# Kernel optimization log

Measured on AMD Instinct MI355X. Metric: run time of the kernel, lower is better.

The kernel has to match this reference:

```python
import math
import jax, jax.numpy as jnp
import numpy as np

H = 8  # num_heads

def _layernorm(x, scale, bias, eps=1e-5):
    m = x.mean(-1, keepdims=True)
    v = x.var(-1, keepdims=True)
    return (x - m) / jnp.sqrt(v + eps) * scale + bias

def setup_inputs() -> dict:
    key = jax.random.key(0)
    ks = jax.random.split(key, 12)
    B, C, P, D, G = 8, 32, 256, 256, 512
    n = jax.random.normal
    return {
        "qz": n(ks[0], (B, C, P, D), dtype=jnp.float32),
        "unary": n(ks[1], (B, C, P, D), dtype=jnp.float32),
        # per-sample condition-instantiated factors; scaled ~1/sqrt(D) so attn logits are sane
        "time_u": n(ks[2], (B, D, D), dtype=jnp.float32) * 0.06,
        "time_v": n(ks[3], (B, D, D), dtype=jnp.float32) * 0.06,
        "channel_u": n(ks[4], (B, D, D), dtype=jnp.float32) * 0.06,
        "channel_v": n(ks[5], (B, D, D), dtype=jnp.float32) * 0.06,
        "topic_binary": n(ks[6], (B, G, D), dtype=jnp.float32) * 0.02,
        "norm_scale": jnp.ones((D,), jnp.float32),
        "norm_bias": jnp.zeros((D,), jnp.float32),
        "gate_w": n(ks[7], (D, D), dtype=jnp.float32) * 0.02,
        "gate_b": jnp.zeros((D,), jnp.float32),
        "out_w1": n(ks[8], (D, D), dtype=jnp.float32) * 0.02,
        "out_b1": jnp.zeros((D,), jnp.float32),
        "out_w2": n(ks[9], (D, D), dtype=jnp.float32) * 0.02,
        "out_b2": jnp.zeros((D,), jnp.float32),
    }

def reference(qz, unary, time_u, time_v, channel_u, channel_v, topic_binary,
              norm_scale, norm_bias, gate_w, gate_b, out_w1, out_b1, out_w2, out_b2):
    B, C, P, D = qz.shape
    R = D // H
    inv_sqrt_r = 1.0 / math.sqrt(R)

    qz_n = _layernorm(qz, norm_scale, norm_bias)

    def heads(x, w):  # [B,C,P,D] x [B,D,D] -> [B,C,P,H,R]
        return jnp.einsum('bcpd,bod->bcpo', x, w).reshape(B, C, P, H, R)

    # --- time-factor message: attention over P within each (b, c, h) ---
    qu = heads(qz_n, time_u).transpose(0, 1, 3, 2, 4)   # [B,C,H,P,R]
    qv = heads(qz_n, time_v).transpose(0, 1, 3, 2, 4)
    attn_t = jax.nn.softmax(jnp.einsum('bchpr,bchqr->bchpq', qu, qv) * inv_sqrt_r, axis=-1)
    m_t = jnp.einsum('bchpq,bcqd->bchpd', attn_t, qz_n).mean(axis=2)  # [B,C,P,D]

    # --- channel-factor message: attention over C within each (b, p, h) ---
    qu = heads(qz_n, channel_u).transpose(0, 2, 3, 1, 4)  # [B,P,H,C,R]
    qv = heads(qz_n, channel_v).transpose(0, 2, 3, 1, 4)
    attn_c = jax.nn.softmax(jnp.einsum('bphcr,bphfr->bphcf', qu, qv) * inv_sqrt_r, axis=-1)
    qzp = qz_n.transpose(0, 2, 1, 3)                      # [B,P,C,D]
    m_c = jnp.einsum('bphcf,bpfd->bphcd', attn_c, qzp).mean(axis=2).transpose(0, 2, 1, 3)

    # --- topic-modeling binary factor with AbsNormalize (relu + L1-normalize) ---
    qg = jax.nn.relu(jnp.einsum('bcpd,bgd->bcpg', qz_n, topic_binary))
    qg = qg / jnp.maximum(qg.sum(axis=-1, keepdims=True), 1e-6)
    m_g = jnp.einsum('bcpg,bgd->bcpd', qg, topic_binary)

    # --- gated residual update ---
    gate = jax.nn.sigmoid(qz @ gate_w.T + gate_b)
    qz2 = gate * qz + (1.0 - gate) * (unary + m_t + m_c + m_g)

    # --- output MLP with shared LayerNorm ---
    h = _layernorm(qz2, norm_scale, norm_bias)
    h = jax.nn.gelu(h @ out_w1.T + out_b1, approximate=False) @ out_w2.T + out_b2
    return qz2 + h
```

## Files before the change

kernel.cpp:

```cpp
#include <hip/hip_runtime.h>
#include <math.h>

namespace {

constexpr float INV_SQRT_R = 0.17677669529663689f;

typedef __attribute__((ext_vector_type(8))) __bf16 bf16x8;
typedef __attribute__((ext_vector_type(4))) float f32x4;

static __device__ __forceinline__ f32x4 MF(bf16x8 a, bf16x8 b, f32x4 c) {
    return __builtin_amdgcn_mfma_f32_16x16x32_bf16(a, b, c, 0, 0, 0);
}


__global__ __launch_bounds__(256) void prep_kernel(
    const float* __restrict__ time_u, const float* __restrict__ time_v,
    const float* __restrict__ chan_u, const float* __restrict__ chan_v,
    const float* __restrict__ topic, const float* __restrict__ gate_w,
    const float* __restrict__ w1, const float* __restrict__ w2,
    __bf16* __restrict__ wtime, __bf16* __restrict__ wchan,
    __bf16* __restrict__ topicb, __bf16* __restrict__ topicTb,
    __bf16* __restrict__ gwF, __bf16* __restrict__ w1F, __bf16* __restrict__ w2F)
{
    __shared__ __bf16 tile[32][34];
    const int blk = blockIdx.x;
    const int t = threadIdx.x;
    if (blk < 2048) {
        const int q = blk >> 9, r = blk & 511;
        const float* src; __bf16* dst; int dstOff;
        if (q == 0)      { src = time_u; dst = wtime; dstOff = 0; }
        else if (q == 1) { src = time_v; dst = wtime; dstOff = 65536; }
        else if (q == 2) { src = chan_u; dst = wchan; dstOff = 0; }
        else             { src = chan_v; dst = wchan; dstOff = 65536; }
        int i = (r * 256 + t) * 4;
        float4 v = *(const float4*)(src + i);
        int o = (i >> 16) * 131072 + dstOff + (i & 65535);
        dst[o + 0] = (__bf16)v.x; dst[o + 1] = (__bf16)v.y;
        dst[o + 2] = (__bf16)v.z; dst[o + 3] = (__bf16)v.w;
    } else if (blk < 3072) {
        int i = ((blk - 2048) * 256 + t) * 4;
        float4 v = *(const float4*)(topic + i);
        topicb[i + 0] = (__bf16)v.x; topicb[i + 1] = (__bf16)v.y;
        topicb[i + 2] = (__bf16)v.z; topicb[i + 3] = (__bf16)v.w;
    } else if (blk < 4096) {
        const int idx = blk - 3072;
        const int r0 = (idx & 15) * 32;
        const int c0 = ((idx >> 4) & 7) * 32;
        const size_t bz = idx >> 7;
        const float* src = topic + bz * 131072;
        __bf16* dst = topicTb + bz * 131072;
        const int tx = t & 31, ty = t >> 5;
        #pragma unroll
        for (int i = 0; i < 32; i += 8)
            tile[ty + i][tx] = (__bf16)src[(size_t)(r0 + ty + i) * 256 + c0 + tx];
        __syncthreads();
        #pragma unroll
        for (int i = 0; i < 32; i += 8)
            dst[(size_t)(c0 + ty + i) * 512 + r0 + tx] = tile[tx][ty + i];
    } else {
        const int w = (blk - 4096) >> 6;
        const int r = (blk - 4096) & 63;
        const float* src = (w == 0) ? gate_w : ((w == 1) ? w1 : w2);
        __bf16* dstB = (w == 0) ? gwF : ((w == 1) ? w1F : w2F);
        int i = (r * 256 + t) * 4;
        float4 v = *(const float4*)(src + i);
        const int n = i >> 8, k = i & 255;
        __bf16* dst = dstB + (k >> 5) * 8192 + n * 32 + (k & 31);
        dst[0] = (__bf16)v.x; dst[1] = (__bf16)v.y; dst[2] = (__bf16)v.z; dst[3] = (__bf16)v.w;
    }
}

__global__ __launch_bounds__(256) void ln_kernel(
    const float* __restrict__ x, const float* __restrict__ sc,
    const float* __restrict__ bi, __bf16* __restrict__ y)
{
    const size_t row = blockIdx.x;
    const int t = threadIdx.x;
    const float v = x[row * 256 + t];
    float s = v, s2 = v * v;
    #pragma unroll
    for (int o = 32; o > 0; o >>= 1) {
        s  += __shfl_xor(s, o);
        s2 += __shfl_xor(s2, o);
    }
    __shared__ float ps[4], ps2[4];
    if ((t & 63) == 0) { ps[t >> 6] = s; ps2[t >> 6] = s2; }
    __syncthreads();
    const float S  = ps[0] + ps[1] + ps[2] + ps[3];
    const float S2 = ps2[0] + ps2[1] + ps2[2] + ps2[3];
    const float mean = S * (1.0f / 256.0f);
    const float var  = S2 * (1.0f / 256.0f) - mean * mean;
    const float inv  = 1.0f / sqrtf(var + 1e-5f);
    y[row * 256 + t] = (__bf16)((v - mean) * inv * sc[t] + bi[t]);
}

__global__ __launch_bounds__(256) void tpose_frag_kernel(
    const __bf16* __restrict__ src, __bf16* __restrict__ dst)
{
    const size_t bz = blockIdx.z;
    src += bz * 65536;
    dst += bz * 65536;
    __shared__ __bf16 tile[32][34];
    const int r0 = blockIdx.x * 32, c0 = blockIdx.y * 32;
    const int tx = threadIdx.x & 31, ty = threadIdx.x >> 5;
    #pragma unroll
    for (int i = 0; i < 32; i += 8)
        tile[ty + i][tx] = src[(size_t)(r0 + ty + i) * 256 + c0 + tx];
    __syncthreads();
    #pragma unroll
    for (int i = 0; i < 32; i += 8)
        dst[(r0 >> 5) * 8192 + (c0 + ty + i) * 32 + tx] = tile[tx][ty + i];
}

__global__ __launch_bounds__(256) void mgemm_kernel(
    const __bf16* __restrict__ A, const __bf16* __restrict__ Bm, __bf16* __restrict__ Cout,
    int K, size_t aStride, size_t bStride,
    size_t s_b, size_t s_c, size_t s_p, size_t s_w, size_t s_h)
{
    const int bb = blockIdx.z;
    const int m0 = blockIdx.x * 64;
    const int n0 = blockIdx.y * 256;
    const __bf16* Ab = A + (size_t)bb * aStride;
    const __bf16* Bb = Bm + (size_t)bb * bStride;
    __shared__ __align__(16) __bf16 As[64][40];
    __shared__ __align__(16) __bf16 Bs[256][40];
    const int t = threadIdx.x;
    const int lane = t & 63;
    const int wid = t >> 6;
    const int l15 = lane & 15, lg = lane >> 4;

    f32x4 acc[4][4] = {};

    for (int k0 = 0; k0 < K; k0 += 32) {
        {
            const int row = t >> 2, k8 = (t & 3) << 3;
            *(bf16x8*)&As[row][k8] = *(const bf16x8*)(Ab + (size_t)(m0 + row) * K + k0 + k8);
        }
        #pragma unroll
        for (int s = 0; s < 4; ++s) {
            const int slot = s * 256 + t;
            const int row = slot >> 2, k8 = (slot & 3) << 3;
            *(bf16x8*)&Bs[row][k8] = *(const bf16x8*)(Bb + (size_t)(n0 + row) * K + k0 + k8);
        }
        __syncthreads();
        bf16x8 af[4], bfr[4];
        #pragma unroll
        for (int i = 0; i < 4; ++i)
            af[i] = *(const bf16x8*)&As[i * 16 + l15][lg * 8];
        #pragma unroll
        for (int j = 0; j < 4; ++j)
            bfr[j] = *(const bf16x8*)&Bs[wid * 64 + j * 16 + l15][lg * 8];
        #pragma unroll
        for (int i = 0; i < 4; ++i)
            #pragma unroll
            for (int j = 0; j < 4; ++j)
                acc[i][j] = MF(af[i], bfr[j], acc[i][j]);
        __syncthreads();
    }

    #pragma unroll
    for (int j = 0; j < 4; ++j) {
        const int n = n0 + wid * 64 + j * 16 + l15;
        const size_t offn = (size_t)(n >> 8) * s_w + (size_t)((n >> 5) & 7) * s_h + (n & 31);
        #pragma unroll
        for (int i = 0; i < 4; ++i) {
            #pragma unroll
            for (int r = 0; r < 4; ++r) {
                const int m = m0 + i * 16 + lg * 4 + r;
                const size_t off = (size_t)bb * s_b + (size_t)(m >> 8) * s_c
                                 + (size_t)(m & 255) * s_p + offn;
                Cout[off] = (__bf16)acc[i][j][r];
            }
        }
    }
}

__global__ __launch_bounds__(256) void time_attn_mt_kernel(
    const __bf16* __restrict__ qu, const __bf16* __restrict__ qv,
    const __bf16* __restrict__ qznTF, __bf16* __restrict__ m_t)
{
    const int bc = blockIdx.x;
    const int p0 = blockIdx.y * 64;
    const __bf16* quB = qu + (size_t)bc * 65536;
    const __bf16* qvB = qv + (size_t)bc * 65536;
    const __bf16* BTF = qznTF + (size_t)bc * 65536;
    __shared__ __align__(16) __bf16 R1[16896];
    __bf16* Us  = R1;
    __bf16* Vs  = R1 + 2560;
    __bf16* aL  = R1;
    const int t = threadIdx.x;
    const int lane = t & 63;
    const int wid = t >> 6;
    const int l15 = lane & 15, lg = lane >> 4;

    f32x4 acc[16] = {};

    for (int h = 0; h < 8; ++h) {
        const __bf16* quH = quB + h * 8192;
        const __bf16* qvH = qvB + h * 8192;
        __syncthreads();
        {
            const int row = t >> 2, k8 = (t & 3) << 3;
            *(bf16x8*)&Us[row * 40 + k8] = *(const bf16x8*)(quH + (size_t)(p0 + row) * 32 + k8);
        }
        #pragma unroll
        for (int i = 0; i < 4; ++i) {
            const int slot = i * 256 + t;
            const int row = slot >> 2, k8 = (slot & 3) << 3;
            *(bf16x8*)&Vs[row * 40 + k8] = *(const bf16x8*)(qvH + (size_t)row * 32 + k8);
        }
        __syncthreads();

        f32x4 s[16];
        bf16x8 a = *(const bf16x8*)&Us[(wid * 16 + l15) * 40 + lg * 8];
        #pragma unroll
        for (int j = 0; j < 16; ++j) {
            bf16x8 bfr = *(const bf16x8*)&Vs[(j * 16 + l15) * 40 + lg * 8];
            s[j] = MF(a, bfr, (f32x4){0.f, 0.f, 0.f, 0.f});
        }

        #pragma unroll
        for (int r = 0; r < 4; ++r) {
            float e[16];
            float sum = 0.0f;
            #pragma unroll
            for (int j = 0; j < 16; ++j) {
                e[j] = __expf(s[j][r] * INV_SQRT_R);
                sum += e[j];
            }
            sum += __shfl_xor(sum, 1);
            sum += __shfl_xor(sum, 2);
            sum += __shfl_xor(sum, 4);
            sum += __shfl_xor(sum, 8);
            const float inv = 0.125f / sum;
            #pragma unroll
            for (int j = 0; j < 16; ++j) acc[j][r] += e[j] * inv;
        }
    }

    __syncthreads();
    #pragma unroll
    for (int r = 0; r < 4; ++r) {
        const int row = wid * 16 + lg * 4 + r;
        #pragma unroll
        for (int j = 0; j < 16; ++j)
            aL[row * 264 + j * 16 + l15] = (__bf16)acc[j][r];
    }
    __syncthreads();

    f32x4 acc2[4][4] = {};
    #pragma unroll
    for (int k0 = 0; k0 < 256; k0 += 32) {
        bf16x8 af[4], bfr[4];
        #pragma unroll
        for (int i = 0; i < 4; ++i)
            af[i] = *(const bf16x8*)&aL[(i * 16 + l15) * 264 + k0 + lg * 8];
        #pragma unroll
        for (int j = 0; j < 4; ++j)
            bfr[j] = *(const bf16x8*)(BTF + (k0 >> 5) * 8192 + (wid * 64 + j * 16 + l15) * 32 + lg * 8);
        #pragma unroll
        for (int i = 0; i < 4; ++i)
            #pragma unroll
            for (int j = 0; j < 4; ++j)
                acc2[i][j] = MF(af[i], bfr[j], acc2[i][j]);
    }
    #pragma unroll
    for (int i = 0; i < 4; ++i)
        #pragma unroll
        for (int j = 0; j < 4; ++j) {
            const int d = wid * 64 + j * 16 + l15;
            #pragma unroll
            for (int r = 0; r < 4; ++r) {
                const int p = p0 + i * 16 + lg * 4 + r;
                m_t[(size_t)bc * 65536 + (size_t)p * 256 + d] = (__bf16)acc2[i][j][r];
            }
        }
}

__global__ __launch_bounds__(256) void chan_fused_kernel(
    const __bf16* __restrict__ quc, const __bf16* __restrict__ qvc,
    const __bf16* __restrict__ qzn, __bf16* __restrict__ m_c)
{
    const int bp = blockIdx.x;
    const int b = bp >> 8, p = bp & 255;
    const __bf16* quB = quc + (size_t)bp * 8192;
    const __bf16* qvB = qvc + (size_t)bp * 8192;
    __shared__ __align__(16) __bf16 QU[20480];
    __shared__ float ab[32 * 33];
    __bf16* qus = QU;
    __bf16* qvs = QU + 10240;
    const int t = threadIdx.x;

    float btr[32];
    #pragma unroll
    for (int f = 0; f < 32; ++f)
        btr[f] = (float)qzn[((size_t)(b * 32 + f) * 256 + p) * 256 + t];

    #pragma unroll
    for (int i = 0; i < 4; ++i) {
        int fi = i * 256 + t;
        int e = fi << 3;
        int h = e >> 10, cc = (e >> 5) & 31, r = e & 31;
        int base = (h * 32 + cc) * 40 + r;
        *(bf16x8*)&qus[base] = *(const bf16x8*)(quB + e);
        *(bf16x8*)&qvs[base] = *(const bf16x8*)(qvB + e);
    }
    __syncthreads();
    const int c = t >> 3, j = t & 7;
    float acc[4] = {0.f, 0.f, 0.f, 0.f};
    for (int h = 0; h < 8; ++h) {
        float qur[32];
        #pragma unroll
        for (int u = 0; u < 4; ++u) {
            bf16x8 q8 = *(const bf16x8*)&qus[(h * 32 + c) * 40 + u * 8];
            #pragma unroll
            for (int e2 = 0; e2 < 8; ++e2) qur[u * 8 + e2] = (float)q8[e2];
        }
        float s[4];
        #pragma unroll
        for (int jj = 0; jj < 4; ++jj) {
            int f = j * 4 + jj;
            float a = 0.f;
            #pragma unroll
            for (int u = 0; u < 4; ++u) {
                bf16x8 v8 = *(const bf16x8*)&qvs[(h * 32 + f) * 40 + u * 8];
                #pragma unroll
                for (int e2 = 0; e2 < 8; ++e2) a += qur[u * 8 + e2] * (float)v8[e2];
            }
            s[jj] = a * INV_SQRT_R;
        }
        float mx = fmaxf(fmaxf(s[0], s[1]), fmaxf(s[2], s[3]));
        mx = fmaxf(mx, __shfl_xor(mx, 1));
        mx = fmaxf(mx, __shfl_xor(mx, 2));
        mx = fmaxf(mx, __shfl_xor(mx, 4));
        float e0x = __expf(s[0] - mx), e1x = __expf(s[1] - mx);
        float e2x = __expf(s[2] - mx), e3x = __expf(s[3] - mx);
        float sum = e0x + e1x + e2x + e3x;
        sum += __shfl_xor(sum, 1);
        sum += __shfl_xor(sum, 2);
        sum += __shfl_xor(sum, 4);
        float inv = 0.125f / sum;
        acc[0] += e0x * inv; acc[1] += e1x * inv; acc[2] += e2x * inv; acc[3] += e3x * inv;
    }
    #pragma unroll
    for (int jj = 0; jj < 4; ++jj) ab[c * 33 + j * 4 + jj] = acc[jj];
    __syncthreads();
    #pragma unroll 2
    for (int c2 = 0; c2 < 32; c2 += 2) {
        float a0 = 0.f, a1 = 0.f;
        #pragma unroll
        for (int f = 0; f < 32; ++f) {
            float v = btr[f];
            a0 += ab[c2 * 33 + f] * v;
            a1 += ab[(c2 + 1) * 33 + f] * v;
        }
        size_t off = ((size_t)(b * 32 + c2) * 256 + p) * 256 + t;
        m_c[off] = (__bf16)a0;
        m_c[off + 65536] = (__bf16)a1;
    }
}

__global__ __launch_bounds__(256, 2) void topic_fused_kernel(
    const __bf16* __restrict__ qzn, const __bf16* __restrict__ topicb,
    const __bf16* __restrict__ topicTb, __bf16* __restrict__ m_g)
{
    const int bb = blockIdx.z;
    const int m0 = blockIdx.x * 32;
    const __bf16* Ab = qzn + (size_t)bb * 2097152;
    const __bf16* B1 = topicb + (size_t)bb * 131072;
    const __bf16* B2 = topicTb + (size_t)bb * 131072;
    __shared__ __align__(16) __bf16 As[32][40];
    __shared__ __align__(16) __bf16 Bs[512][40];
    __shared__ __align__(16) __bf16 Ps[32][520];
    __shared__ float rsInv[32];
    const int t = threadIdx.x;
    const int lane = t & 63, wid = t >> 6;
    const int l15 = lane & 15, lg = lane >> 4;

    f32x4 acc[2][8] = {};
    for (int k0 = 0; k0 < 256; k0 += 32) {
        if (t < 128) {
            const int row = t >> 2, k8 = (t & 3) << 3;
            *(bf16x8*)&As[row][k8] = *(const bf16x8*)(Ab + (size_t)(m0 + row) * 256 + k0 + k8);
        }
        #pragma unroll
        for (int s = 0; s < 8; ++s) {
            const int slot = s * 256 + t;
            const int row = slot >> 2, k8 = (slot & 3) << 3;
            *(bf16x8*)&Bs[row][k8] = *(const bf16x8*)(B1 + (size_t)row * 256 + k0 + k8);
        }
        __syncthreads();
        bf16x8 af0 = *(const bf16x8*)&As[l15][lg * 8];
        bf16x8 af1 = *(const bf16x8*)&As[16 + l15][lg * 8];
        #pragma unroll
        for (int j = 0; j < 8; ++j) {
            bf16x8 b8 = *(const bf16x8*)&Bs[wid * 128 + j * 16 + l15][lg * 8];
            acc[0][j] = MF(af0, b8, acc[0][j]);
            acc[1][j] = MF(af1, b8, acc[1][j]);
        }
        __syncthreads();
    }
    #pragma unroll
    for (int i = 0; i < 2; ++i)
        #pragma unroll
        for (int j = 0; j < 8; ++j) {
            const int n = wid * 128 + j * 16 + l15;
            #pragma unroll
            for (int r = 0; r < 4; ++r)
                Ps[i * 16 + lg * 4 + r][n] = (__bf16)fmaxf(acc[i][j][r], 0.0f);
        }
    __syncthreads();
    {
        const int row = t >> 3, seg = t & 7;
        float s = 0.0f;
        #pragma unroll
        for (int u = 0; u < 8; ++u) {
            bf16x8 v = *(const bf16x8*)&Ps[row][seg * 64 + u * 8];
            #pragma unroll
            for (int e = 0; e < 8; ++e) s += (float)v[e];
        }
        s += __shfl_xor(s, 1);
        s += __shfl_xor(s, 2);
        s += __shfl_xor(s, 4);
        if (seg == 0) rsInv[row] = 1.0f / fmaxf(s, 1e-6f);
    }
    __syncthreads();
    f32x4 acc2[2][4] = {};
    for (int k0 = 0; k0 < 512; k0 += 32) {
        #pragma unroll
        for (int s = 0; s < 4; ++s) {
            const int slot = s * 256 + t;
            const int row = slot >> 2, k8 = (slot & 3) << 3;
            *(bf16x8*)&Bs[row][k8] = *(const bf16x8*)(B2 + (size_t)row * 512 + k0 + k8);
        }
        __syncthreads();
        bf16x8 af0 = *(const bf16x8*)&Ps[l15][k0 + lg * 8];
        bf16x8 af1 = *(const bf16x8*)&Ps[16 + l15][k0 + lg * 8];
        #pragma unroll
        for (int j = 0; j < 4; ++j) {
            bf16x8 b8 = *(const bf16x8*)&Bs[wid * 64 + j * 16 + l15][lg * 8];
            acc2[0][j] = MF(af0, b8, acc2[0][j]);
            acc2[1][j] = MF(af1, b8, acc2[1][j]);
        }
        __syncthreads();
    }
    #pragma unroll
    for (int i = 0; i < 2; ++i)
        #pragma unroll
        for (int j = 0; j < 4; ++j) {
            const int n = wid * 64 + j * 16 + l15;
            #pragma unroll
            for (int r = 0; r < 4; ++r) {
                const int ml = i * 16 + lg * 4 + r;
                m_g[(size_t)bb * 2097152 + (size_t)(m0 + ml) * 256 + n]
                    = (__bf16)(acc2[i][j][r] * rsInv[ml]);
            }
        }
}

__global__ __launch_bounds__(256) void mega_kernel(
    const float* __restrict__ qz, const float* __restrict__ unary,
    const __bf16* __restrict__ m_t, const __bf16* __restrict__ m_c,
    const __bf16* __restrict__ m_g,
    const __bf16* __restrict__ gwF, const float* __restrict__ gate_b,
    const __bf16* __restrict__ w1F, const float* __restrict__ b1,
    const __bf16* __restrict__ w2F, const float* __restrict__ b2,
    const float* __restrict__ nsc, const float* __restrict__ nbi,
    float* __restrict__ outp)
{
    const int m0 = blockIdx.x * 64;
    __shared__ __align__(16) __bf16 hL[64][264];
    __shared__ float lnp[64][8];
    const int t = threadIdx.x;
    const int lane = t & 63, wid = t >> 6;
    const int l15 = lane & 15, lg = lane >> 4;

    #pragma unroll
    for (int s = 0; s < 8; ++s) {
        const int slot = s * 256 + t;
        const int row = slot >> 5;
        const int k8 = (slot & 31) << 3;
        const float* src = qz + (size_t)(m0 + row) * 256 + k8;
        float4 v0 = *(const float4*)src;
        float4 v1 = *(const float4*)(src + 4);
        bf16x8 pk;
        pk[0] = (__bf16)v0.x; pk[1] = (__bf16)v0.y; pk[2] = (__bf16)v0.z; pk[3] = (__bf16)v0.w;
        pk[4] = (__bf16)v1.x; pk[5] = (__bf16)v1.y; pk[6] = (__bf16)v1.z; pk[7] = (__bf16)v1.w;
        *(bf16x8*)&hL[row][k8] = pk;
    }
    __syncthreads();

    f32x4 acc[4][4] = {};
    #pragma unroll
    for (int k0 = 0; k0 < 256; k0 += 32) {
        bf16x8 af[4], bfr[4];
        #pragma unroll
        for (int i = 0; i < 4; ++i) af[i] = *(const bf16x8*)&hL[i * 16 + l15][k0 + lg * 8];
        #pragma unroll
        for (int j = 0; j < 4; ++j)
            bfr[j] = *(const bf16x8*)(gwF + (k0 >> 5) * 8192 + (wid * 64 + j * 16 + l15) * 32 + lg * 8);
        #pragma unroll
        for (int i = 0; i < 4; ++i)
            #pragma unroll
            for (int j = 0; j < 4; ++j)
                acc[i][j] = MF(af[i], bfr[j], acc[i][j]);
    }

    f32x4 z2[4][4];
    #pragma unroll
    for (int i = 0; i < 4; ++i) {
        #pragma unroll
        for (int r = 0; r < 4; ++r) {
            const int rr = i * 16 + lg * 4 + r;
            float s = 0.0f, s2 = 0.0f;
            #pragma unroll
            for (int j = 0; j < 4; ++j) {
                const int n = wid * 64 + j * 16 + l15;
                const size_t off = (size_t)(m0 + rr) * 256 + n;
                float g = 1.0f / (1.0f + __expf(-(acc[i][j][r] + gate_b[n])));
                float rest = unary[off] + (float)m_t[off] + (float)m_c[off] + (float)m_g[off];
                float v = g * (float)hL[rr][n] + (1.0f - g) * rest;
                z2[i][j][r] = v;
                s += v; s2 += v * v;
            }
            s  += __shfl_xor(s, 1);  s  += __shfl_xor(s, 2);
            s  += __shfl_xor(s, 4);  s  += __shfl_xor(s, 8);
            s2 += __shfl_xor(s2, 1); s2 += __shfl_xor(s2, 2);
            s2 += __shfl_xor(s2, 4); s2 += __shfl_xor(s2, 8);
            if (l15 == 0) {
                lnp[rr][wid * 2 + 0] = s;
                lnp[rr][wid * 2 + 1] = s2;
            }
        }
    }
    __syncthreads();
    #pragma unroll
    for (int i = 0; i < 4; ++i) {
        #pragma unroll
        for (int r = 0; r < 4; ++r) {
            const int rr = i * 16 + lg * 4 + r;
            float S  = lnp[rr][0] + lnp[rr][2] + lnp[rr][4] + lnp[rr][6];
            float S2 = lnp[rr][1] + lnp[rr][3] + lnp[rr][5] + lnp[rr][7];
            float mean = S * (1.0f / 256.0f);
            float var  = S2 * (1.0f / 256.0f) - mean * mean;
            float inv  = 1.0f / sqrtf(var + 1e-5f);
            #pragma unroll
            for (int j = 0; j < 4; ++j) {
                const int n = wid * 64 + j * 16 + l15;
                hL[rr][n] = (__bf16)((z2[i][j][r] - mean) * inv * nsc[n] + nbi[n]);
            }
        }
    }
    __syncthreads();

    f32x4 acc2[4][4] = {};
    #pragma unroll
    for (int k0 = 0; k0 < 256; k0 += 32) {
        bf16x8 af[4], bfr[4];
        #pragma unroll
        for (int i = 0; i < 4; ++i) af[i] = *(const bf16x8*)&hL[i * 16 + l15][k0 + lg * 8];
        #pragma unroll
        for (int j = 0; j < 4; ++j)
            bfr[j] = *(const bf16x8*)(w1F + (k0 >> 5) * 8192 + (wid * 64 + j * 16 + l15) * 32 + lg * 8);
        #pragma unroll
        for (int i = 0; i < 4; ++i)
            #pragma unroll
            for (int j = 0; j < 4; ++j)
                acc2[i][j] = MF(af[i], bfr[j], acc2[i][j]);
    }
    __syncthreads();
    #pragma unroll
    for (int i = 0; i < 4; ++i)
        #pragma unroll
        for (int j = 0; j < 4; ++j) {
            const int n = wid * 64 + j * 16 + l15;
            const float bn = b1[n];
            #pragma unroll
            for (int r = 0; r < 4; ++r) {
                float x = acc2[i][j][r] + bn;
                hL[i * 16 + lg * 4 + r][n] = (__bf16)(0.5f * x * (1.0f + erff(x * 0.7071067811865475f)));
            }
        }
    __syncthreads();

    f32x4 acc3[4][4] = {};
    #pragma unroll
    for (int k0 = 0; k0 < 256; k0 += 32) {
        bf16x8 af[4], bfr[4];
        #pragma unroll
        for (int i = 0; i < 4; ++i) af[i] = *(const bf16x8*)&hL[i * 16 + l15][k0 + lg * 8];
        #pragma unroll
        for (int j = 0; j < 4; ++j)
            bfr[j] = *(const bf16x8*)(w2F + (k0 >> 5) * 8192 + (wid * 64 + j * 16 + l15) * 32 + lg * 8);
        #pragma unroll
        for (int i = 0; i < 4; ++i)
            #pragma unroll
            for (int j = 0; j < 4; ++j)
                acc3[i][j] = MF(af[i], bfr[j], acc3[i][j]);
    }
    #pragma unroll
    for (int i = 0; i < 4; ++i)
        #pragma unroll
        for (int j = 0; j < 4; ++j) {
            const int n = wid * 64 + j * 16 + l15;
            const float bn = b2[n];
            #pragma unroll
            for (int r = 0; r < 4; ++r) {
                const size_t off = (size_t)(m0 + i * 16 + lg * 4 + r) * 256 + n;
                outp[off] = z2[i][j][r] + acc3[i][j][r] + bn;
            }
        }
}

}

extern "C" void kernel_launch(void* const* d_in, const int* in_sizes, int n_in,
                              void* d_out, int out_size, void* d_ws, size_t ws_size,
                              hipStream_t stream)
{
    (void)in_sizes; (void)n_in; (void)out_size; (void)ws_size;
    const float* qz     = (const float*)d_in[0];
    const float* unary  = (const float*)d_in[1];
    const float* time_u = (const float*)d_in[2];
    const float* time_v = (const float*)d_in[3];
    const float* chan_u = (const float*)d_in[4];
    const float* chan_v = (const float*)d_in[5];
    const float* topic  = (const float*)d_in[6];
    const float* nsc    = (const float*)d_in[7];
    const float* nbi    = (const float*)d_in[8];
    const float* gate_w = (const float*)d_in[9];
    const float* gate_b = (const float*)d_in[10];
    const float* w1     = (const float*)d_in[11];
    const float* b1     = (const float*)d_in[12];
    const float* w2     = (const float*)d_in[13];
    const float* b2     = (const float*)d_in[14];

    char* base = (char*)d_ws;
    __bf16* qzn_b  = (__bf16*)base;
    __bf16* pool   = (__bf16*)(base + (32ull << 20));
    __bf16* wtime  = pool;
    __bf16* wchan  = pool + 1048576;
    __bf16* topicb = pool + 2097152;
    __bf16* topicTb= pool + 3145728;
    __bf16* gwF    = pool + 4194304;
    __bf16* w1F    = pool + 4259840;
    __bf16* w2F    = pool + 4325376;
    __bf16* Blo    = (__bf16*)(base + (64ull << 20));
    __bf16* Bhi    = (__bf16*)(base + (96ull << 20));
    __bf16* qu_t   = Blo;
    __bf16* qv_t   = Bhi;
    __bf16* qu_c   = Blo;
    __bf16* qv_c   = Bhi;
    __bf16* m_g    = Blo;
    __bf16* qznTF  = (__bf16*)(base + (128ull << 20));
    __bf16* m_c    = qznTF;
    __bf16* m_t    = (__bf16*)(base + (160ull << 20));
    float*  OUTF   = (float*)d_out;

    dim3 blk(256);

    prep_kernel<<<4288, blk, 0, stream>>>(
        time_u, time_v, chan_u, chan_v, topic, gate_w, w1, w2,
        wtime, wchan, topicb, topicTb, gwF, w1F, w2F);

    ln_kernel<<<65536, blk, 0, stream>>>(qz, nsc, nbi, qzn_b);
    tpose_frag_kernel<<<dim3(8, 8, 256), blk, 0, stream>>>(qzn_b, qznTF);

    mgemm_kernel<<<dim3(128, 2, 8), blk, 0, stream>>>(
        qzn_b, wtime, qu_t, 256, 2097152, 131072,
        2097152, 65536, 32, 16777216, 8192);

    time_attn_mt_kernel<<<dim3(256, 4), blk, 0, stream>>>(qu_t, qv_t, qznTF, m_t);

    mgemm_kernel<<<dim3(128, 2, 8), blk, 0, stream>>>(
        qzn_b, wchan, qu_c, 256, 2097152, 131072,
        2097152, 32, 8192, 16777216, 1024);

    chan_fused_kernel<<<2048, blk, 0, stream>>>(qu_c, qv_c, qzn_b, m_c);

    topic_fused_kernel<<<dim3(256, 1, 8), blk, 0, stream>>>(qzn_b, topicb, topicTb, m_g);

    mega_kernel<<<1024, blk, 0, stream>>>(
        qz, unary, m_t, m_c, m_g,
        gwF, gate_b, w1F, b1, w2F, b2, nsc, nbi, OUTF);
}
```

Measured before the change: 483.6 us.

## Fuse time attention and channel projection GEMM into one interleaved launch

```diff
diff --git a/kernel.cpp b/kernel.cpp
--- a/kernel.cpp
+++ b/kernel.cpp
@@ -175,106 +175,168 @@
     }
 }
 
-__global__ __launch_bounds__(256) void time_attn_mt_kernel(
+__global__ __launch_bounds__(256) void mid_kernel(
     const __bf16* __restrict__ qu, const __bf16* __restrict__ qv,
-    const __bf16* __restrict__ qznTF, __bf16* __restrict__ m_t)
-{
-    const int bc = blockIdx.x;
-    const int p0 = blockIdx.y * 64;
-    const __bf16* quB = qu + (size_t)bc * 65536;
-    const __bf16* qvB = qv + (size_t)bc * 65536;
-    const __bf16* BTF = qznTF + (size_t)bc * 65536;
-    __shared__ __align__(16) __bf16 R1[16896];
-    __bf16* Us  = R1;
-    __bf16* Vs  = R1 + 2560;
-    __bf16* aL  = R1;
+    const __bf16* __restrict__ qznTF, __bf16* __restrict__ m_t,
+    const __bf16* __restrict__ qzn, const __bf16* __restrict__ wchan,
+    __bf16* __restrict__ quc_out)
+{
+    __shared__ __align__(16) __bf16 SH[16896];
     const int t = threadIdx.x;
     const int lane = t & 63;
     const int wid = t >> 6;
     const int l15 = lane & 15, lg = lane >> 4;
-
-    f32x4 acc[16] = {};
-
-    for (int h = 0; h < 8; ++h) {
-        const __bf16* quH = quB + h * 8192;
-        const __bf16* qvH = qvB + h * 8192;
-        __syncthreads();
-        {
-            const int row = t >> 2, k8 = (t & 3) << 3;
-            *(bf16x8*)&Us[row * 40 + k8] = *(const bf16x8*)(quH + (size_t)(p0 + row) * 32 + k8);
-        }
-        #pragma unroll
-        for (int i = 0; i < 4; ++i) {
-            const int slot = i * 256 + t;
-            const int row = slot >> 2, k8 = (slot & 3) << 3;
-            *(bf16x8*)&Vs[row * 40 + k8] = *(const bf16x8*)(qvH + (size_t)row * 32 + k8);
-        }
-        __syncthreads();
-
-        f32x4 s[16];
-        bf16x8 a = *(const bf16x8*)&Us[(wid * 16 + l15) * 40 + lg * 8];
-        #pragma unroll
-        for (int j = 0; j < 16; ++j) {
-            bf16x8 bfr = *(const bf16x8*)&Vs[(j * 16 + l15) * 40 + lg * 8];
-            s[j] = MF(a, bfr, (f32x4){0.f, 0.f, 0.f, 0.f});
-        }
-
+    const int g = blockIdx.x / 3;
+    const int rb = blockIdx.x % 3;
+
+    if (rb == 0) {
+        const int bc = g & 255;
+        const int p0 = (g >> 8) * 64;
+        const __bf16* quB = qu + (size_t)bc * 65536;
+        const __bf16* qvB = qv + (size_t)bc * 65536;
+        const __bf16* BTF = qznTF + (size_t)bc * 65536;
+        __bf16* Us = SH;
+        __bf16* Vs = SH + 2560;
+        __bf16* aL = SH;
+
+        f32x4 acc[16] = {};
+
+        for (int h = 0; h < 8; ++h) {
+            const __bf16* quH = quB + h * 8192;
+            const __bf16* qvH = qvB + h * 8192;
+            __syncthreads();
+            {
+                const int row = t >> 2, k8 = (t & 3) << 3;
+                *(bf16x8*)&Us[row * 40 + k8] = *(const bf16x8*)(quH + (size_t)(p0 + row) * 32 + k8);
+            }
+            #pragma unroll
+            for (int i = 0; i < 4; ++i) {
+                const int slot = i * 256 + t;
+                const int row = slot >> 2, k8 = (slot & 3) << 3;
+                *(bf16x8*)&Vs[row * 40 + k8] = *(const bf16x8*)(qvH + (size_t)row * 32 + k8);
+            }
+            __syncthreads();
+
+            f32x4 s[16];
+            bf16x8 a = *(const bf16x8*)&Us[(wid * 16 + l15) * 40 + lg * 8];
+            #pragma unroll
+            for (int j = 0; j < 16; ++j) {
+                bf16x8 bfr = *(const bf16x8*)&Vs[(j * 16 + l15) * 40 + lg * 8];
+                s[j] = MF(a, bfr, (f32x4){0.f, 0.f, 0.f, 0.f});
+            }
+
+            #pragma unroll
+            for (int r = 0; r < 4; ++r) {
+                float e[16];
+                float sum = 0.0f;
+                #pragma unroll
+                for (int j = 0; j < 16; ++j) {
+                    e[j] = __expf(s[j][r] * INV_SQRT_R);
+                    sum += e[j];
+                }
+                sum += __shfl_xor(sum, 1);
+                sum += __shfl_xor(sum, 2);
+                sum += __shfl_xor(sum, 4);
+                sum += __shfl_xor(sum, 8);
+                const float inv = 0.125f / sum;
+                #pragma unroll
+                for (int j = 0; j < 16; ++j) acc[j][r] += e[j] * inv;
+            }
+        }
+
+        __syncthreads();
         #pragma unroll
         for (int r = 0; r < 4; ++r) {
-            float e[16];
-            float sum = 0.0f;
-            #pragma unroll
-            for (int j = 0; j < 16; ++j) {
-                e[j] = __expf(s[j][r] * INV_SQRT_R);
-                sum += e[j];
-            }
-            sum += __shfl_xor(sum, 1);
-            sum += __shfl_xor(sum, 2);
-            sum += __shfl_xor(sum, 4);
-            sum += __shfl_xor(sum, 8);
-            const float inv = 0.125f / sum;
-            #pragma unroll
-            for (int j = 0; j < 16; ++j) acc[j][r] += e[j] * inv;
-        }
-    }
-
-    __syncthreads();
-    #pragma unroll
-    for (int r = 0; r < 4; ++r) {
-        const int row = wid * 16 + lg * 4 + r;
-        #pragma unroll
-        for (int j = 0; j < 16; ++j)
-            aL[row * 264 + j * 16 + l15] = (__bf16)acc[j][r];
-    }
-    __syncthreads();
-
-    f32x4 acc2[4][4] = {};
-    #pragma unroll
-    for (int k0 = 0; k0 < 256; k0 += 32) {
-        bf16x8 af[4], bfr[4];
+            const int row = wid * 16 + lg * 4 + r;
+            #pragma unroll
+            for (int j = 0; j < 16; ++j)
+                aL[row * 264 + j * 16 + l15] = (__bf16)acc[j][r];
+        }
+        __syncthreads();
+
+        f32x4 acc2[4][4] = {};
+        #pragma unroll
+        for (int k0 = 0; k0 < 256; k0 += 32) {
+            bf16x8 af[4], bfr[4];
+            #pragma unroll
+            for (int i = 0; i < 4; ++i)
+                af[i] = *(const bf16x8*)&aL[(i * 16 + l15) * 264 + k0 + lg * 8];
+            #pragma unroll
+            for (int j = 0; j < 4; ++j)
+                bfr[j] = *(const bf16x8*)(BTF + (k0 >> 5) * 8192 + (wid * 64 + j * 16 + l15) * 32 + lg * 8);
+            #pragma unroll
+            for (int i = 0; i < 4; ++i)
+                #pragma unroll
+                for (int j = 0; j < 4; ++j)
+                    acc2[i][j] = MF(af[i], bfr[j], acc2[i][j]);
+        }
         #pragma unroll
         for (int i = 0; i < 4; ++i)
-            af[i] = *(const bf16x8*)&aL[(i * 16 + l15) * 264 + k0 + lg * 8];
-        #pragma unroll
-        for (int j = 0; j < 4; ++j)
-            bfr[j] = *(const bf16x8*)(BTF + (k0 >> 5) * 8192 + (wid * 64 + j * 16 + l15) * 32 + lg * 8);
-        #pragma unroll
-        for (int i = 0; i < 4; ++i)
+            #pragma unroll
+            for (int j = 0; j < 4; ++j) {
+                const int d = wid * 64 + j * 16 + l15;
+                #pragma unroll
+                for (int r = 0; r < 4; ++r) {
+                    const int p = p0 + i * 16 + lg * 4 + r;
+                    m_t[(size_t)bc * 65536 + (size_t)p * 256 + d] = (__bf16)acc2[i][j][r];
+                }
+            }
+    } else {
+        const int idx = g * 2 + (rb - 1);
+        const int bb = idx >> 8;
+        const int rr = idx & 255;
+        const int m0 = (rr & 127) * 64;
+        const int n0 = (rr >> 7) * 256;
+        const __bf16* Ab = qzn + (size_t)bb * 2097152;
+        const __bf16* Bb = wchan + (size_t)bb * 131072;
+        __bf16* As = SH;
+        __bf16* Bs = SH + 2560;
+
+        f32x4 acc[4][4] = {};
+
+        for (int k0 = 0; k0 < 256; k0 += 32) {
+            {
+                const int row = t >> 2, k8 = (t & 3) << 3;
+                *(bf16x8*)&As[row * 40 + k8] = *(const bf16x8*)(Ab + (size_t)(m0 + row) * 256 + k0 + k8);
+            }
+            #pragma unroll
+            for (int s = 0; s < 4; ++s) {
+                const int slot = s * 256 + t;
+                const int row = slot >> 2, k8 = (slot & 3) << 3;
+                *(bf16x8*)&Bs[row * 40 + k8] = *(const bf16x8*)(Bb + (size_t)(n0 + row) * 256 + k0 + k8);
+            }
+            __syncthreads();
+            bf16x8 af[4], bfr[4];
+            #pragma unroll
+            for (int i = 0; i < 4; ++i)
+                af[i] = *(const bf16x8*)&As[(i * 16 + l15) * 40 + lg * 8];
             #pragma unroll
             for (int j = 0; j < 4; ++j)
-                acc2[i][j] = MF(af[i], bfr[j], acc2[i][j]);
-    }
-    #pragma unroll
-    for (int i = 0; i < 4; ++i)
+                bfr[j] = *(const bf16x8*)&Bs[(wid * 64 + j * 16 + l15) * 40 + lg * 8];
+            #pragma unroll
+            for (int i = 0; i < 4; ++i)
+                #pragma unroll
+                for (int j = 0; j < 4; ++j)
+                    acc[i][j] = MF(af[i], bfr[j], acc[i][j]);
+            __syncthreads();
+        }
+
         #pragma unroll
         for (int j = 0; j < 4; ++j) {
-            const int d = wid * 64 + j * 16 + l15;
-            #pragma unroll
-            for (int r = 0; r < 4; ++r) {
-                const int p = p0 + i * 16 + lg * 4 + r;
-                m_t[(size_t)bc * 65536 + (size_t)p * 256 + d] = (__bf16)acc2[i][j][r];
-            }
-        }
+            const int n = n0 + wid * 64 + j * 16 + l15;
+            const size_t offn = (size_t)(n >> 8) * 16777216 + (size_t)((n >> 5) & 7) * 1024 + (n & 31);
+            #pragma unroll
+            for (int i = 0; i < 4; ++i) {
+                #pragma unroll
+                for (int r = 0; r < 4; ++r) {
+                    const int m = m0 + i * 16 + lg * 4 + r;
+                    const size_t off = (size_t)bb * 2097152 + (size_t)(m >> 8) * 32
+                                     + (size_t)(m & 255) * 8192 + offn;
+                    quc_out[off] = (__bf16)acc[i][j][r];
+                }
+            }
+        }
+    }
 }
 
 __global__ __launch_bounds__(256) void chan_fused_kernel(
@@ -649,12 +711,11 @@
     __bf16* Bhi    = (__bf16*)(base + (96ull << 20));
     __bf16* qu_t   = Blo;
     __bf16* qv_t   = Bhi;
-    __bf16* qu_c   = Blo;
-    __bf16* qv_c   = Bhi;
     __bf16* m_g    = Blo;
     __bf16* qznTF  = (__bf16*)(base + (128ull << 20));
     __bf16* m_c    = qznTF;
     __bf16* m_t    = (__bf16*)(base + (160ull << 20));
+    __bf16* quc    = (__bf16*)d_out;
     float*  OUTF   = (float*)d_out;
 
     dim3 blk(256);
@@ -670,13 +731,10 @@
         qzn_b, wtime, qu_t, 256, 2097152, 131072,
         2097152, 65536, 32, 16777216, 8192);
 
-    time_attn_mt_kernel<<<dim3(256, 4), blk, 0, stream>>>(qu_t, qv_t, qznTF, m_t);
-
-    mgemm_kernel<<<dim3(128, 2, 8), blk, 0, stream>>>(
-        qzn_b, wchan, qu_c, 256, 2097152, 131072,
-        2097152, 32, 8192, 16777216, 1024);
-
-    chan_fused_kernel<<<2048, blk, 0, stream>>>(qu_c, qv_c, qzn_b, m_c);
+    mid_kernel<<<3072, blk, 0, stream>>>(
+        qu_t, qv_t, qznTF, m_t, qzn_b, wchan, quc);
+
+    chan_fused_kernel<<<2048, blk, 0, stream>>>(quc, quc + 16777216, qzn_b, m_c);
 
     topic_fused_kernel<<<dim3(256, 1, 8), blk, 0, stream>>>(qzn_b, topicb, topicTb, m_g);
 
```

Measured after the change: 581.4 us. 20.2% more time.
